# Kernel tuning notes

Measured on AMD Instinct MI355X. Metric: run time of the kernel, lower is better.

Reference implementation:

```python
import jax, jax.numpy as jnp
import numpy as np

B, T, D, H = 2, 2048, 1024, 16  # batch, seq, n_embed, n_head


def setup_inputs() -> dict:
    key = jax.random.key(0)
    ks = jax.random.split(key, 5)
    scale = 1.0 / np.sqrt(D)
    return {
        "x": jax.random.normal(ks[0], (B, T, D), dtype=jnp.float32),
        "Wq": jax.random.normal(ks[1], (D, D), dtype=jnp.float32) * scale,
        "Wk": jax.random.normal(ks[2], (D, D), dtype=jnp.float32) * scale,
        "Wv": jax.random.normal(ks[3], (D, D), dtype=jnp.float32) * scale,
        "Wo": jax.random.normal(ks[4], (D, D), dtype=jnp.float32) * scale,
    }


def reference(x, Wq, Wk, Wv, Wo):
    b, t, d = x.shape
    hd = d // H  # head_dim
    # projections -> [B, H, T, hd]
    q = (x @ Wq).reshape(b, t, H, hd).transpose(0, 2, 1, 3)
    k = (x @ Wk).reshape(b, t, H, hd).transpose(0, 2, 1, 3)
    v = (x @ Wv).reshape(b, t, H, hd).transpose(0, 2, 1, 3)
    # scaled scores [B, H, T, T] with causal mask
    e = jnp.einsum("bhqd,bhkd->bhqk", q, k) * (1.0 / np.sqrt(hd))
    causal = jnp.tril(jnp.ones((t, t), dtype=bool))
    e = jnp.where(causal[None, None], e, jnp.finfo(e.dtype).min)
    alpha = jax.nn.softmax(e, axis=-1)
    # attention output -> [B, T, D]
    attn = jnp.einsum("bhqk,bhkd->bhqd", alpha, v)
    attn = attn.transpose(0, 2, 1, 3).reshape(b, t, d)
    return attn @ Wo
```

## Files before the change

### kernel.cpp

```cpp
#include <hip/hip_runtime.h>
#include <hip/hip_bf16.h>
#include <math.h>


#define Bsz  2
#define Tseq 2048
#define Dm   1024
#define NH   16
#define HD   64

typedef short bf16x8 __attribute__((ext_vector_type(8)));
typedef float floatx4 __attribute__((ext_vector_type(4)));

__device__ __forceinline__ unsigned short f2bf(float f) {
    __hip_bfloat16 h = __float2bfloat16(f);
    return *reinterpret_cast<unsigned short*>(&h);
}

__device__ __forceinline__ unsigned short f2bf_fast(float f) {
    unsigned int u = __builtin_bit_cast(unsigned int, f);
    return (unsigned short)((u + 0x8000u) >> 16);
}

__device__ __forceinline__ void lds16(unsigned short* lds, const unsigned short* g) {
    __builtin_amdgcn_global_load_lds(
        (const __attribute__((address_space(1))) void*)g,
        (__attribute__((address_space(3))) void*)lds, 16, 0, 0);
}

__global__ __launch_bounds__(256) void prep(const float* __restrict__ x,
                                            const float* __restrict__ W0,
                                            const float* __restrict__ W1,
                                            const float* __restrict__ W2,
                                            const float* __restrict__ W3,
                                            unsigned short* __restrict__ xb,
                                            unsigned short* __restrict__ T0,
                                            unsigned short* __restrict__ T1,
                                            unsigned short* __restrict__ T2,
                                            unsigned short* __restrict__ T3) {
    __shared__ float t[64][65];
    const int z = blockIdx.z;
    if (z >= 4) {
        const int bi = (z - 4) * 256 + blockIdx.y * 16 + blockIdx.x;
        const size_t i = (size_t)bi * 256 + threadIdx.x;
        const float4 v = ((const float4*)x)[i];
        ushort4 o;
        o.x = f2bf(v.x); o.y = f2bf(v.y); o.z = f2bf(v.z); o.w = f2bf(v.w);
        ((ushort4*)xb)[i] = o;
        return;
    }
    const float* W = (z == 0) ? W0 : (z == 1) ? W1 : (z == 2) ? W2 : W3;
    unsigned short* T = (z == 0) ? T0 : (z == 1) ? T1 : (z == 2) ? T2 : T3;
    const int k0 = blockIdx.y * 64, n0 = blockIdx.x * 64;
    const int row = threadIdx.x >> 6, col = threadIdx.x & 63;
#pragma unroll
    for (int p = 0; p < 16; ++p)
        t[p * 4 + row][col] = W[(size_t)(k0 + p * 4 + row) * Dm + n0 + col];
    __syncthreads();
#pragma unroll
    for (int p = 0; p < 16; ++p)
        T[(size_t)(n0 + p * 4 + row) * Dm + k0 + col] = f2bf(t[col][p * 4 + row]);
}

__device__ __forceinline__ void gemm128_mainloop(const unsigned short* __restrict__ A,
                                                 const unsigned short* __restrict__ Bt,
                                                 int K, int m0, int n0,
                                                 unsigned short* As, unsigned short* Bs,
                                                 floatx4 acc[4][4]) {
    const int tid = threadIdx.x;
    const int lane = tid & 63, wave = tid >> 6;
    const int l15 = lane & 15, quad = lane >> 4;
    const int wm = (wave >> 1) * 64, wn = (wave & 1) * 64;

    const int qsw = (quad ^ ((l15 >> 1) & 3)) * 8;

    for (int k0 = 0; k0 < K; k0 += 32) {
        __syncthreads();
#pragma unroll
        for (int c = 0; c < 2; ++c) {
            const int idx = c * 256 + tid;
            const int row = idx >> 2, kc = (idx & 3) * 8;
            const int sk = ((idx & 3) ^ ((row >> 1) & 3)) * 8;
            lds16(&As[row * 32 + kc], A + (size_t)(m0 + row) * K + k0 + sk);
            lds16(&Bs[row * 32 + kc], Bt + (size_t)(n0 + row) * K + k0 + sk);
        }
        __syncthreads();
        bf16x8 af[4], bfr[4];
#pragma unroll
        for (int i = 0; i < 4; ++i)
            af[i] = *(const bf16x8*)&As[(wm + i * 16 + l15) * 32 + qsw];
#pragma unroll
        for (int j = 0; j < 4; ++j)
            bfr[j] = *(const bf16x8*)&Bs[(wn + j * 16 + l15) * 32 + qsw];
#pragma unroll
        for (int i = 0; i < 4; ++i)
#pragma unroll
            for (int j = 0; j < 4; ++j)
                acc[i][j] = __builtin_amdgcn_mfma_f32_16x16x32_bf16(af[i], bfr[j], acc[i][j], 0, 0, 0);
    }
}

__global__ __launch_bounds__(256) void gemm_qkv(const unsigned short* __restrict__ xb,
                                                const unsigned short* __restrict__ Wqt,
                                                const unsigned short* __restrict__ Wkt,
                                                const unsigned short* __restrict__ Wvt,
                                                unsigned short* __restrict__ Qb,
                                                unsigned short* __restrict__ Kb,
                                                unsigned short* __restrict__ VbT) {
    __shared__ unsigned short As[128 * 32];
    __shared__ unsigned short Bs[128 * 32];
    const int z = blockIdx.z;
    const unsigned short* Bt = (z == 0) ? Wqt : (z == 1) ? Wkt : Wvt;
    const float scale = (z == 0) ? (0.125f * 1.4426950408889634f) : 1.0f;

    const int wg = blockIdx.x + 8 * blockIdx.y;
    const int m_idx = (wg & 7) * 4 + (wg >> 6);
    const int n_idx = (wg >> 3) & 7;
    const int m0 = m_idx * 128, n0 = n_idx * 128;

    floatx4 acc[4][4];
#pragma unroll
    for (int i = 0; i < 4; ++i)
#pragma unroll
        for (int j = 0; j < 4; ++j) acc[i][j] = (floatx4){0.f, 0.f, 0.f, 0.f};

    gemm128_mainloop(xb, Bt, Dm, m0, n0, As, Bs, acc);

    const int lane = threadIdx.x & 63, wave = threadIdx.x >> 6;
    const int l15 = lane & 15, quad = lane >> 4;
    const int wm = (wave >> 1) * 64, wn = (wave & 1) * 64;

    if (z == 2) {
#pragma unroll
        for (int i = 0; i < 4; ++i)
#pragma unroll
            for (int j = 0; j < 4; ++j) {
                const int col = n0 + wn + j * 16 + l15;
                const int hh = col >> 6, dd = col & 63;
                const int tok = m0 + wm + i * 16 + quad * 4;
                const int bb = tok >> 11, tl = tok & (Tseq - 1);
                ushort4 o;
                o.x = f2bf(acc[i][j][0]); o.y = f2bf(acc[i][j][1]);
                o.z = f2bf(acc[i][j][2]); o.w = f2bf(acc[i][j][3]);
                *(ushort4*)&VbT[((size_t)((bb * NH + hh) * HD + dd)) * Tseq + tl] = o;
            }
        return;
    }
    unsigned short* C = (z == 0) ? Qb : Kb;
#pragma unroll
    for (int i = 0; i < 4; ++i)
#pragma unroll
        for (int j = 0; j < 4; ++j)
#pragma unroll
            for (int r = 0; r < 4; ++r) {
                const int row = m0 + wm + i * 16 + quad * 4 + r;
                const int col = n0 + wn + j * 16 + l15;
                C[(size_t)row * Dm + col] = f2bf(acc[i][j][r] * scale);
            }
}

__global__ __launch_bounds__(256) void gemm_out(const unsigned short* __restrict__ Yb,
                                                const unsigned short* __restrict__ Wot,
                                                float* __restrict__ out) {
    __shared__ unsigned short As[128 * 32];
    __shared__ unsigned short Bs[64 * 32];
    const int wg = blockIdx.x + 16 * blockIdx.y;
    const int m_idx = (wg & 7) * 4 + (wg >> 7);
    const int n_idx = (wg >> 3) & 15;
    const int m0 = m_idx * 128, n0 = n_idx * 64;
    const int tid = threadIdx.x;
    const int lane = tid & 63, wave = tid >> 6;
    const int l15 = lane & 15, quad = lane >> 4;
    const int wm = (wave >> 1) * 64, wn = (wave & 1) * 32;
    const int qsw = (quad ^ ((l15 >> 1) & 3)) * 8;

    floatx4 acc[4][2];
#pragma unroll
    for (int i = 0; i < 4; ++i)
#pragma unroll
        for (int j = 0; j < 2; ++j) acc[i][j] = (floatx4){0.f, 0.f, 0.f, 0.f};

    for (int k0 = 0; k0 < Dm; k0 += 32) {
        __syncthreads();
#pragma unroll
        for (int c = 0; c < 2; ++c) {
            const int idx = c * 256 + tid;
            const int row = idx >> 2, kc = (idx & 3) * 8;
            const int sk = ((idx & 3) ^ ((row >> 1) & 3)) * 8;
            lds16(&As[row * 32 + kc], Yb + (size_t)(m0 + row) * Dm + k0 + sk);
        }
        {
            const int row = tid >> 2, kc = (tid & 3) * 8;
            const int sk = ((tid & 3) ^ ((row >> 1) & 3)) * 8;
            lds16(&Bs[row * 32 + kc], Wot + (size_t)(n0 + row) * Dm + k0 + sk);
        }
        __syncthreads();
        bf16x8 af[4], bfr[2];
#pragma unroll
        for (int i = 0; i < 4; ++i)
            af[i] = *(const bf16x8*)&As[(wm + i * 16 + l15) * 32 + qsw];
#pragma unroll
        for (int j = 0; j < 2; ++j)
            bfr[j] = *(const bf16x8*)&Bs[(wn + j * 16 + l15) * 32 + qsw];
#pragma unroll
        for (int i = 0; i < 4; ++i)
#pragma unroll
            for (int j = 0; j < 2; ++j)
                acc[i][j] = __builtin_amdgcn_mfma_f32_16x16x32_bf16(af[i], bfr[j], acc[i][j], 0, 0, 0);
    }

#pragma unroll
    for (int i = 0; i < 4; ++i)
#pragma unroll
        for (int j = 0; j < 2; ++j)
#pragma unroll
            for (int r = 0; r < 4; ++r) {
                const int row = m0 + wm + i * 16 + quad * 4 + r;
                const int col = n0 + wn + j * 16 + l15;
                out[(size_t)row * Dm + col] = acc[i][j][r];
            }
}

__global__ __launch_bounds__(256) void attn_mfma(const unsigned short* __restrict__ Qb,
                                                 const unsigned short* __restrict__ Kb,
                                                 const unsigned short* __restrict__ VbT,
                                                 unsigned short* __restrict__ Yb) {
    const int bh = blockIdx.x;
    const int b = bh >> 4;
    const int h = bh & 15;
    const int qt = 31 - blockIdx.y;
    const int tid = threadIdx.x;
    const int wave = tid >> 6;
    const int lane = tid & 63;
    const int l15 = lane & 15;
    const int quad = lane >> 4;

    __shared__ unsigned short Ks0[64][32];
    __shared__ unsigned short Ks1[64][32];
    __shared__ unsigned short Vt0[64][32];
    __shared__ unsigned short Vt1[64][32];
    __shared__ unsigned short Ps[4][16][72];

    const size_t tok0 = (size_t)b * Tseq;
    const int colh = h * HD;

    const int qrow = qt * 64 + wave * 16;

    const unsigned short* qptr = Qb + (tok0 + qrow + l15) * Dm + colh + quad * 8;
    const bf16x8 qf0 = *(const bf16x8*)(qptr);
    const bf16x8 qf1 = *(const bf16x8*)(qptr + 32);

    float l_lane = 0.f;
    floatx4 o_acc[4];
#pragma unroll
    for (int t = 0; t < 4; ++t) o_acc[t] = (floatx4){0.f, 0.f, 0.f, 0.f};

    const int srow = tid >> 2;
    const int sc8 = (tid & 3) * 8;
    const int ssw = ((tid & 3) ^ ((srow >> 1) & 3)) * 8;
    const int qsw = (quad ^ ((l15 >> 1) & 3)) * 8;

    const unsigned short* krow = Kb + (tok0 + srow) * Dm + colh;
    const unsigned short* vrow = VbT + (size_t)bh * HD * Tseq + (size_t)srow * Tseq;

    const int niter = qt + 1;
    for (int it = 0; it < niter; ++it) {
        const int k0 = it * 64;
        __syncthreads();
        lds16(&Ks0[srow][sc8], krow + ssw);
        lds16(&Ks1[srow][sc8], krow + 32 + ssw);
        lds16(&Vt0[srow][sc8], vrow + ssw);
        lds16(&Vt1[srow][sc8], vrow + 32 + ssw);
        krow += 64 * Dm;
        vrow += 64;
        __syncthreads();

        floatx4 sf[4];
        __builtin_amdgcn_s_setprio(1);
#pragma unroll
        for (int t = 0; t < 4; ++t) {
            floatx4 c = (floatx4){0.f, 0.f, 0.f, 0.f};
            const bf16x8 kb0 = *(const bf16x8*)&Ks0[t * 16 + l15][qsw];
            const bf16x8 kb1 = *(const bf16x8*)&Ks1[t * 16 + l15][qsw];
            c = __builtin_amdgcn_mfma_f32_16x16x32_bf16(kb0, qf0, c, 0, 0, 0);
            c = __builtin_amdgcn_mfma_f32_16x16x32_bf16(kb1, qf1, c, 0, 0, 0);
            sf[t] = c;
        }
        __builtin_amdgcn_s_setprio(0);

        if (k0 + 63 > qrow) {
            const int ql = qrow + l15;
#pragma unroll
            for (int t = 0; t < 4; ++t)
#pragma unroll
                for (int r = 0; r < 4; ++r) {
                    const int kl = k0 + t * 16 + quad * 4 + r;
                    if (kl > ql) sf[t][r] = -1.0e30f;
                }
        }

#pragma unroll
        for (int t = 0; t < 4; ++t) {
            float p0 = __builtin_amdgcn_exp2f(sf[t][0]);
            float p1 = __builtin_amdgcn_exp2f(sf[t][1]);
            float p2 = __builtin_amdgcn_exp2f(sf[t][2]);
            float p3 = __builtin_amdgcn_exp2f(sf[t][3]);
            l_lane += (p0 + p1) + (p2 + p3);
            unsigned int w0, w1;
            asm("v_cvt_pk_bf16_f32 %0, %1, %2" : "=v"(w0) : "v"(p0), "v"(p1));
            asm("v_cvt_pk_bf16_f32 %0, %1, %2" : "=v"(w1) : "v"(p2), "v"(p3));
            uint2 o; o.x = w0; o.y = w1;
            *(uint2*)&Ps[wave][l15][t * 16 + quad * 4] = o;
        }

        const bf16x8 pa0 = *(const bf16x8*)&Ps[wave][l15][quad * 8];
        const bf16x8 pa1 = *(const bf16x8*)&Ps[wave][l15][32 + quad * 8];
        __builtin_amdgcn_s_setprio(1);
#pragma unroll
        for (int t = 0; t < 4; ++t) {
            const bf16x8 vb0 = *(const bf16x8*)&Vt0[t * 16 + l15][qsw];
            const bf16x8 vb1 = *(const bf16x8*)&Vt1[t * 16 + l15][qsw];
            o_acc[t] = __builtin_amdgcn_mfma_f32_16x16x32_bf16(pa0, vb0, o_acc[t], 0, 0, 0);
            o_acc[t] = __builtin_amdgcn_mfma_f32_16x16x32_bf16(pa1, vb1, o_acc[t], 0, 0, 0);
        }
        __builtin_amdgcn_s_setprio(0);
    }

    l_lane += __shfl_xor(l_lane, 16);
    l_lane += __shfl_xor(l_lane, 32);
    const float inv_q = 1.0f / l_lane;
    float inv_r[4];
#pragma unroll
    for (int r = 0; r < 4; ++r)
        inv_r[r] = __shfl(inv_q, (lane & 48) | (quad * 4 + r));
#pragma unroll
    for (int t = 0; t < 4; ++t)
#pragma unroll
        for (int r = 0; r < 4; ++r) {
            const int q = qrow + quad * 4 + r;
            Yb[(tok0 + q) * Dm + colh + t * 16 + l15] = f2bf(o_acc[t][r] * inv_r[r]);
        }
}

extern "C" void kernel_launch(void* const* d_in, const int* in_sizes, int n_in,
                              void* d_out, int out_size, void* d_ws, size_t ws_size,
                              hipStream_t stream) {
    const float* x  = (const float*)d_in[0];
    const float* Wq = (const float*)d_in[1];
    const float* Wk = (const float*)d_in[2];
    const float* Wv = (const float*)d_in[3];
    const float* Wo = (const float*)d_in[4];
    float* out = (float*)d_out;

    const int M = Bsz * Tseq;
    char* ws = (char*)d_ws;
    unsigned short* xb  = (unsigned short*)(ws);
    unsigned short* Wqt = (unsigned short*)(ws + (((size_t)8)  << 20));
    unsigned short* Wkt = (unsigned short*)(ws + (((size_t)10) << 20));
    unsigned short* Wvt = (unsigned short*)(ws + (((size_t)12) << 20));
    unsigned short* Wot = (unsigned short*)(ws + (((size_t)14) << 20));
    unsigned short* Qb  = (unsigned short*)(ws + (((size_t)16) << 20));
    unsigned short* Kb  = (unsigned short*)(ws + (((size_t)24) << 20));
    unsigned short* VbT = (unsigned short*)(ws + (((size_t)32) << 20));
    unsigned short* Yb  = (unsigned short*)(ws + (((size_t)40) << 20));

    dim3 blk(256);
    hipLaunchKernelGGL(prep, dim3(16, 16, 20), blk, 0, stream,
                       x, Wq, Wk, Wv, Wo, xb, Wqt, Wkt, Wvt, Wot);

    hipLaunchKernelGGL(gemm_qkv, dim3(Dm / 128, M / 128, 3), blk, 0, stream,
                       xb, Wqt, Wkt, Wvt, Qb, Kb, VbT);

    hipLaunchKernelGGL(attn_mfma, dim3(Bsz * NH, 32), blk, 0, stream, Qb, Kb, VbT, Yb);

    hipLaunchKernelGGL(gemm_out, dim3(Dm / 64, M / 128), blk, 0, stream, Yb, Wot, out);
}
```

Before: 169.1 us.

## Process 128 query rows per attention block, 32 per wave, to reuse K/V tiles

The attention kernel now handles a 128-row query tile per block, with each wave owning two 16-row query groups. Every K/V tile loaded into LDS is therefore used by twice as many query rows, which halves K/V global traffic and the per-tile barrier cost. The trade-off is half as many blocks (less parallelism and coarser causal load balancing), more registers per wave, and waves that idle on tiles past their causal limit while still taking part in the barriers.

```diff
diff --git a/kernel.cpp b/kernel.cpp
--- a/kernel.cpp
+++ b/kernel.cpp
@@ -15,11 +15,6 @@
 __device__ __forceinline__ unsigned short f2bf(float f) {
     __hip_bfloat16 h = __float2bfloat16(f);
     return *reinterpret_cast<unsigned short*>(&h);
-}
-
-__device__ __forceinline__ unsigned short f2bf_fast(float f) {
-    unsigned int u = __builtin_bit_cast(unsigned int, f);
-    return (unsigned short)((u + 0x8000u) >> 16);
 }
 
 __device__ __forceinline__ void lds16(unsigned short* lds, const unsigned short* g) {
@@ -228,7 +223,7 @@
     const int bh = blockIdx.x;
     const int b = bh >> 4;
     const int h = bh & 15;
-    const int qt = 31 - blockIdx.y;
+    const int qt = 15 - blockIdx.y;
     const int tid = threadIdx.x;
     const int wave = tid >> 6;
     const int lane = tid & 63;
@@ -239,21 +234,26 @@
     __shared__ unsigned short Ks1[64][32];
     __shared__ unsigned short Vt0[64][32];
     __shared__ unsigned short Vt1[64][32];
-    __shared__ unsigned short Ps[4][16][72];
+    __shared__ unsigned short Ps[4][32][72];
 
     const size_t tok0 = (size_t)b * Tseq;
     const int colh = h * HD;
 
-    const int qrow = qt * 64 + wave * 16;
-
-    const unsigned short* qptr = Qb + (tok0 + qrow + l15) * Dm + colh + quad * 8;
-    const bf16x8 qf0 = *(const bf16x8*)(qptr);
-    const bf16x8 qf1 = *(const bf16x8*)(qptr + 32);
-
-    float l_lane = 0.f;
-    floatx4 o_acc[4];
-#pragma unroll
-    for (int t = 0; t < 4; ++t) o_acc[t] = (floatx4){0.f, 0.f, 0.f, 0.f};
+    const int qrow = qt * 128 + wave * 32;
+
+    const unsigned short* qbase = Qb + (tok0 + qrow) * Dm + colh;
+    const bf16x8 qf00 = *(const bf16x8*)(qbase + (size_t)l15 * Dm + quad * 8);
+    const bf16x8 qf01 = *(const bf16x8*)(qbase + (size_t)l15 * Dm + 32 + quad * 8);
+    const bf16x8 qf10 = *(const bf16x8*)(qbase + (size_t)(16 + l15) * Dm + quad * 8);
+    const bf16x8 qf11 = *(const bf16x8*)(qbase + (size_t)(16 + l15) * Dm + 32 + quad * 8);
+
+    float l0 = 0.f, l1 = 0.f;
+    floatx4 o0[4], o1[4];
+#pragma unroll
+    for (int t = 0; t < 4; ++t) {
+        o0[t] = (floatx4){0.f, 0.f, 0.f, 0.f};
+        o1[t] = (floatx4){0.f, 0.f, 0.f, 0.f};
+    }
 
     const int srow = tid >> 2;
     const int sc8 = (tid & 3) * 8;
@@ -263,7 +263,7 @@
     const unsigned short* krow = Kb + (tok0 + srow) * Dm + colh;
     const unsigned short* vrow = VbT + (size_t)bh * HD * Tseq + (size_t)srow * Tseq;
 
-    const int niter = qt + 1;
+    const int niter = 2 * qt + 2;
     for (int it = 0; it < niter; ++it) {
         const int k0 = it * 64;
         __syncthreads();
@@ -275,16 +275,22 @@
         vrow += 64;
         __syncthreads();
 
-        floatx4 sf[4];
+        if (k0 > qrow + 31) continue;
+
+        floatx4 sf0[4], sf1[4];
         __builtin_amdgcn_s_setprio(1);
 #pragma unroll
         for (int t = 0; t < 4; ++t) {
-            floatx4 c = (floatx4){0.f, 0.f, 0.f, 0.f};
             const bf16x8 kb0 = *(const bf16x8*)&Ks0[t * 16 + l15][qsw];
             const bf16x8 kb1 = *(const bf16x8*)&Ks1[t * 16 + l15][qsw];
-            c = __builtin_amdgcn_mfma_f32_16x16x32_bf16(kb0, qf0, c, 0, 0, 0);
-            c = __builtin_amdgcn_mfma_f32_16x16x32_bf16(kb1, qf1, c, 0, 0, 0);
-            sf[t] = c;
+            floatx4 c0 = (floatx4){0.f, 0.f, 0.f, 0.f};
+            floatx4 c1 = (floatx4){0.f, 0.f, 0.f, 0.f};
+            c0 = __builtin_amdgcn_mfma_f32_16x16x32_bf16(kb0, qf00, c0, 0, 0, 0);
+            c0 = __builtin_amdgcn_mfma_f32_16x16x32_bf16(kb1, qf01, c0, 0, 0, 0);
+            c1 = __builtin_amdgcn_mfma_f32_16x16x32_bf16(kb0, qf10, c1, 0, 0, 0);
+            c1 = __builtin_amdgcn_mfma_f32_16x16x32_bf16(kb1, qf11, c1, 0, 0, 0);
+            sf0[t] = c0;
+            sf1[t] = c1;
         }
         __builtin_amdgcn_s_setprio(0);
 
@@ -295,50 +301,84 @@
 #pragma unroll
                 for (int r = 0; r < 4; ++r) {
                     const int kl = k0 + t * 16 + quad * 4 + r;
-                    if (kl > ql) sf[t][r] = -1.0e30f;
+                    if (kl > ql) sf0[t][r] = -1.0e30f;
                 }
         }
+        if (k0 + 63 > qrow + 16) {
+            const int ql = qrow + 16 + l15;
+#pragma unroll
+            for (int t = 0; t < 4; ++t)
+#pragma unroll
+                for (int r = 0; r < 4; ++r) {
+                    const int kl = k0 + t * 16 + quad * 4 + r;
+                    if (kl > ql) sf1[t][r] = -1.0e30f;
+                }
+        }
 
 #pragma unroll
         for (int t = 0; t < 4; ++t) {
-            float p0 = __builtin_amdgcn_exp2f(sf[t][0]);
-            float p1 = __builtin_amdgcn_exp2f(sf[t][1]);
-            float p2 = __builtin_amdgcn_exp2f(sf[t][2]);
-            float p3 = __builtin_amdgcn_exp2f(sf[t][3]);
-            l_lane += (p0 + p1) + (p2 + p3);
+            float p0 = __builtin_amdgcn_exp2f(sf0[t][0]);
+            float p1 = __builtin_amdgcn_exp2f(sf0[t][1]);
+            float p2 = __builtin_amdgcn_exp2f(sf0[t][2]);
+            float p3 = __builtin_amdgcn_exp2f(sf0[t][3]);
+            l0 += (p0 + p1) + (p2 + p3);
             unsigned int w0, w1;
             asm("v_cvt_pk_bf16_f32 %0, %1, %2" : "=v"(w0) : "v"(p0), "v"(p1));
             asm("v_cvt_pk_bf16_f32 %0, %1, %2" : "=v"(w1) : "v"(p2), "v"(p3));
             uint2 o; o.x = w0; o.y = w1;
             *(uint2*)&Ps[wave][l15][t * 16 + quad * 4] = o;
         }
-
-        const bf16x8 pa0 = *(const bf16x8*)&Ps[wave][l15][quad * 8];
-        const bf16x8 pa1 = *(const bf16x8*)&Ps[wave][l15][32 + quad * 8];
+#pragma unroll
+        for (int t = 0; t < 4; ++t) {
+            float p0 = __builtin_amdgcn_exp2f(sf1[t][0]);
+            float p1 = __builtin_amdgcn_exp2f(sf1[t][1]);
+            float p2 = __builtin_amdgcn_exp2f(sf1[t][2]);
+            float p3 = __builtin_amdgcn_exp2f(sf1[t][3]);
+            l1 += (p0 + p1) + (p2 + p3);
+            unsigned int w0, w1;
+            asm("v_cvt_pk_bf16_f32 %0, %1, %2" : "=v"(w0) : "v"(p0), "v"(p1));
+            asm("v_cvt_pk_bf16_f32 %0, %1, %2" : "=v"(w1) : "v"(p2), "v"(p3));
+            uint2 o; o.x = w0; o.y = w1;
+            *(uint2*)&Ps[wave][16 + l15][t * 16 + quad * 4] = o;
+        }
+
+        const bf16x8 pa00 = *(const bf16x8*)&Ps[wave][l15][qsw? quad * 8 : quad * 8];
+        const bf16x8 pa01 = *(const bf16x8*)&Ps[wave][l15][32 + quad * 8];
+        const bf16x8 pa10 = *(const bf16x8*)&Ps[wave][16 + l15][quad * 8];
+        const bf16x8 pa11 = *(const bf16x8*)&Ps[wave][16 + l15][32 + quad * 8];
         __builtin_amdgcn_s_setprio(1);
 #pragma unroll
         for (int t = 0; t < 4; ++t) {
             const bf16x8 vb0 = *(const bf16x8*)&Vt0[t * 16 + l15][qsw];
             const bf16x8 vb1 = *(const bf16x8*)&Vt1[t * 16 + l15][qsw];
-            o_acc[t] = __builtin_amdgcn_mfma_f32_16x16x32_bf16(pa0, vb0, o_acc[t], 0, 0, 0);
-            o_acc[t] = __builtin_amdgcn_mfma_f32_16x16x32_bf16(pa1, vb1, o_acc[t], 0, 0, 0);
+            o0[t] = __builtin_amdgcn_mfma_f32_16x16x32_bf16(pa00, vb0, o0[t], 0, 0, 0);
+            o0[t] = __builtin_amdgcn_mfma_f32_16x16x32_bf16(pa01, vb1, o0[t], 0, 0, 0);
+            o1[t] = __builtin_amdgcn_mfma_f32_16x16x32_bf16(pa10, vb0, o1[t], 0, 0, 0);
+            o1[t] = __builtin_amdgcn_mfma_f32_16x16x32_bf16(pa11, vb1, o1[t], 0, 0, 0);
         }
         __builtin_amdgcn_s_setprio(0);
     }
 
-    l_lane += __shfl_xor(l_lane, 16);
-    l_lane += __shfl_xor(l_lane, 32);
-    const float inv_q = 1.0f / l_lane;
-    float inv_r[4];
-#pragma unroll
-    for (int r = 0; r < 4; ++r)
-        inv_r[r] = __shfl(inv_q, (lane & 48) | (quad * 4 + r));
+    l0 += __shfl_xor(l0, 16);
+    l0 += __shfl_xor(l0, 32);
+    l1 += __shfl_xor(l1, 16);
+    l1 += __shfl_xor(l1, 32);
+    const float inv0 = 1.0f / l0;
+    const float inv1 = 1.0f / l1;
+    float inv0_r[4], inv1_r[4];
+#pragma unroll
+    for (int r = 0; r < 4; ++r) {
+        inv0_r[r] = __shfl(inv0, (lane & 48) | (quad * 4 + r));
+        inv1_r[r] = __shfl(inv1, (lane & 48) | (quad * 4 + r));
+    }
 #pragma unroll
     for (int t = 0; t < 4; ++t)
 #pragma unroll
         for (int r = 0; r < 4; ++r) {
-            const int q = qrow + quad * 4 + r;
-            Yb[(tok0 + q) * Dm + colh + t * 16 + l15] = f2bf(o_acc[t][r] * inv_r[r]);
+            const int q0 = qrow + quad * 4 + r;
+            const int q1 = qrow + 16 + quad * 4 + r;
+            Yb[(tok0 + q0) * Dm + colh + t * 16 + l15] = f2bf(o0[t][r] * inv0_r[r]);
+            Yb[(tok0 + q1) * Dm + colh + t * 16 + l15] = f2bf(o1[t][r] * inv1_r[r]);
         }
 }
 
@@ -371,7 +411,7 @@
     hipLaunchKernelGGL(gemm_qkv, dim3(Dm / 128, M / 128, 3), blk, 0, stream,
                        xb, Wqt, Wkt, Wvt, Qb, Kb, VbT);
 
-    hipLaunchKernelGGL(attn_mfma, dim3(Bsz * NH, 32), blk, 0, stream, Qb, Kb, VbT, Yb);
+    hipLaunchKernelGGL(attn_mfma, dim3(Bsz * NH, 16), blk, 0, stream, Qb, Kb, VbT, Yb);
 
     hipLaunchKernelGGL(gemm_out, dim3(Dm / 64, M / 128), blk, 0, stream, Yb, Wot, out);
 }
```

Result: slower. 183.4 us (+8.4%).

## Split long causal query tiles across two KV chunks with a merge kernel

Applied to the files above, without the earlier changes.

The attention grid grows from 32 to 48 query-tile slots per head. Query tiles 16–31 are each split into two blocks: one covers KV tiles 0–15 and the other covers the rest. Each half writes an unnormalized bf16 partial output and its row sums to scratch space reused from the xb and Wqt buffers. A new merge kernel adds the two partials and normalizes them into Yb. The aim is to shorten the longest per-block causal loop and remove tail imbalance across CUs. The cost is an extra kernel launch, extra global traffic, and a bf16 rounding of the partial outputs.

```diff
diff --git a/kernel.cpp b/kernel.cpp
--- a/kernel.cpp
+++ b/kernel.cpp
@@ -17,9 +17,9 @@
     return *reinterpret_cast<unsigned short*>(&h);
 }
 
-__device__ __forceinline__ unsigned short f2bf_fast(float f) {
-    unsigned int u = __builtin_bit_cast(unsigned int, f);
-    return (unsigned short)((u + 0x8000u) >> 16);
+__device__ __forceinline__ float bf2f(unsigned short u) {
+    unsigned int x = ((unsigned int)u) << 16;
+    return __builtin_bit_cast(float, x);
 }
 
 __device__ __forceinline__ void lds16(unsigned short* lds, const unsigned short* g) {
@@ -224,11 +224,20 @@
 __global__ __launch_bounds__(256) void attn_mfma(const unsigned short* __restrict__ Qb,
                                                  const unsigned short* __restrict__ Kb,
                                                  const unsigned short* __restrict__ VbT,
-                                                 unsigned short* __restrict__ Yb) {
+                                                 unsigned short* __restrict__ Yb,
+                                                 unsigned short* __restrict__ Op,
+                                                 float* __restrict__ lp) {
     const int bh = blockIdx.x;
     const int b = bh >> 4;
     const int h = bh & 15;
-    const int qt = 31 - blockIdx.y;
+    const int y = blockIdx.y;
+
+    int qt, itStart, itEnd, chunk;
+    bool partial;
+    if (y < 16)      { qt = 16 + y; chunk = 0; itStart = 0;  itEnd = 16;     partial = true;  }
+    else if (y < 32) { qt = 47 - y; chunk = 1; itStart = 16; itEnd = qt + 1; partial = true;  }
+    else             { qt = 47 - y; chunk = 0; itStart = 0;  itEnd = qt + 1; partial = false; }
+
     const int tid = threadIdx.x;
     const int wave = tid >> 6;
     const int lane = tid & 63;
@@ -260,11 +269,10 @@
     const int ssw = ((tid & 3) ^ ((srow >> 1) & 3)) * 8;
     const int qsw = (quad ^ ((l15 >> 1) & 3)) * 8;
 
-    const unsigned short* krow = Kb + (tok0 + srow) * Dm + colh;
-    const unsigned short* vrow = VbT + (size_t)bh * HD * Tseq + (size_t)srow * Tseq;
-
-    const int niter = qt + 1;
-    for (int it = 0; it < niter; ++it) {
+    const unsigned short* krow = Kb + (tok0 + itStart * 64 + srow) * Dm + colh;
+    const unsigned short* vrow = VbT + (size_t)bh * HD * Tseq + (size_t)srow * Tseq + itStart * 64;
+
+    for (int it = itStart; it < itEnd; ++it) {
         const int k0 = it * 64;
         __syncthreads();
         lds16(&Ks0[srow][sc8], krow + ssw);
@@ -328,6 +336,20 @@
 
     l_lane += __shfl_xor(l_lane, 16);
     l_lane += __shfl_xor(l_lane, 32);
+
+    if (partial) {
+        const size_t slot = ((size_t)(bh * 16 + (qt - 16)) * 2 + chunk);
+        unsigned short* Opb = Op + slot * 4096;
+        float* lpb = lp + slot * 64;
+#pragma unroll
+        for (int t = 0; t < 4; ++t)
+#pragma unroll
+            for (int r = 0; r < 4; ++r)
+                Opb[(wave * 16 + quad * 4 + r) * 64 + t * 16 + l15] = f2bf(o_acc[t][r]);
+        if (quad == 0) lpb[wave * 16 + l15] = l_lane;
+        return;
+    }
+
     const float inv_q = 1.0f / l_lane;
     float inv_r[4];
 #pragma unroll
@@ -340,6 +362,39 @@
             const int q = qrow + quad * 4 + r;
             Yb[(tok0 + q) * Dm + colh + t * 16 + l15] = f2bf(o_acc[t][r] * inv_r[r]);
         }
+}
+
+__global__ __launch_bounds__(256) void attn_merge(const unsigned short* __restrict__ Op,
+                                                  const float* __restrict__ lp,
+                                                  unsigned short* __restrict__ Yb) {
+    const int bh = blockIdx.x >> 4;
+    const int qh = blockIdx.x & 15;
+    const int qt = 16 + qh;
+    const int b = bh >> 4, h = bh & 15;
+    const int tid = threadIdx.x;
+    const int q = tid >> 2;
+    const int d0 = (tid & 3) * 16;
+
+    const size_t slot = ((size_t)(bh * 16 + qh) * 2);
+    const unsigned short* O0 = Op + slot * 4096;
+    const unsigned short* O1 = O0 + 4096;
+    const float* l0 = lp + slot * 64;
+    const float* l1 = l0 + 64;
+
+    const float inv = 1.0f / (l0[q] + l1[q]);
+    unsigned short* dst = Yb + ((size_t)b * Tseq + qt * 64 + q) * Dm + h * HD + d0;
+    const int src = q * 64 + d0;
+#pragma unroll
+    for (int c = 0; c < 4; ++c) {
+        const ushort4 a = *(const ushort4*)&O0[src + c * 4];
+        const ushort4 bb = *(const ushort4*)&O1[src + c * 4];
+        ushort4 o;
+        o.x = f2bf((bf2f(a.x) + bf2f(bb.x)) * inv);
+        o.y = f2bf((bf2f(a.y) + bf2f(bb.y)) * inv);
+        o.z = f2bf((bf2f(a.z) + bf2f(bb.z)) * inv);
+        o.w = f2bf((bf2f(a.w) + bf2f(bb.w)) * inv);
+        *(ushort4*)&dst[c * 4] = o;
+    }
 }
 
 extern "C" void kernel_launch(void* const* d_in, const int* in_sizes, int n_in,
@@ -363,6 +418,8 @@
     unsigned short* Kb  = (unsigned short*)(ws + (((size_t)24) << 20));
     unsigned short* VbT = (unsigned short*)(ws + (((size_t)32) << 20));
     unsigned short* Yb  = (unsigned short*)(ws + (((size_t)40) << 20));
+    unsigned short* Op = xb;
+    float* lp = (float*)Wqt;
 
     dim3 blk(256);
     hipLaunchKernelGGL(prep, dim3(16, 16, 20), blk, 0, stream,
@@ -371,7 +428,10 @@
     hipLaunchKernelGGL(gemm_qkv, dim3(Dm / 128, M / 128, 3), blk, 0, stream,
                        xb, Wqt, Wkt, Wvt, Qb, Kb, VbT);
 
-    hipLaunchKernelGGL(attn_mfma, dim3(Bsz * NH, 32), blk, 0, stream, Qb, Kb, VbT, Yb);
+    hipLaunchKernelGGL(attn_mfma, dim3(Bsz * NH, 48), blk, 0, stream,
+                       Qb, Kb, VbT, Yb, Op, lp);
+
+    hipLaunchKernelGGL(attn_merge, dim3(Bsz * NH * 16), blk, 0, stream, Op, lp, Yb);
 
     hipLaunchKernelGGL(gemm_out, dim3(Dm / 64, M / 128), blk, 0, stream, Yb, Wot, out);
 }
```

Result: no change. 168.8 us (-0.2%).
